# Kernel optimization log

Hardware: AMD Instinct MI355X
Metric: run time of the kernel (lower is better)

Reference implementation:

```python
import jax, jax.numpy as jnp
import numpy as np

N = 100000
E = 3200000
G = 64  # number of graphs


def _lin_params(key, fan_in, fan_out):
    k1, k2 = jax.random.split(key)
    bound = 1.0 / np.sqrt(fan_in)
    W = jax.random.uniform(k1, (fan_in, fan_out), jnp.float32, -bound, bound)
    b = jax.random.uniform(k2, (fan_out,), jnp.float32, -bound, bound)
    return W, b


def setup_inputs() -> dict:
    key = jax.random.key(0)
    ks = jax.random.split(key, 12)
    x = jax.random.normal(ks[0], (N, 3), jnp.float32)
    edge_index = jax.random.randint(ks[1], (2, E), 0, N, jnp.int32)
    batch = jnp.sort(jax.random.randint(ks[2], (N,), 0, G, jnp.int32))
    # conv1: in=3, heads=4, out_channels=16, concat=True -> 64
    Wq1, bq1 = _lin_params(ks[3], 3, 64)
    Wk1, bk1 = _lin_params(ks[4], 3, 64)
    Wv1, bv1 = _lin_params(ks[5], 3, 64)
    Ws1, bs1 = _lin_params(ks[6], 3, 64)
    # conv2: in=64, heads=1, out_channels=6, concat=False -> 6
    Wq2, bq2 = _lin_params(ks[7], 64, 6)
    Wk2, bk2 = _lin_params(ks[8], 64, 6)
    Wv2, bv2 = _lin_params(ks[9], 64, 6)
    Ws2, bs2 = _lin_params(ks[10], 64, 6)
    return dict(x=x, edge_index=edge_index, batch=batch,
                Wq1=Wq1, bq1=bq1, Wk1=Wk1, bk1=bk1, Wv1=Wv1, bv1=bv1, Ws1=Ws1, bs1=bs1,
                Wq2=Wq2, bq2=bq2, Wk2=Wk2, bk2=bk2, Wv2=Wv2, bv2=bv2, Ws2=Ws2, bs2=bs2)


def transformer_conv(x, src, dst, Wq, bq, Wk, bk, Wv, bv, Ws, bs, heads, d, concat):
    n = x.shape[0]
    q = (x @ Wq + bq).reshape(n, heads, d)
    k = (x @ Wk + bk).reshape(n, heads, d)
    v = (x @ Wv + bv).reshape(n, heads, d)
    # per-edge attention logits: query at target, key at source  [E, H]
    logits = jnp.einsum('ehd,ehd->eh', q[dst], k[src]) / jnp.sqrt(jnp.float32(d))
    # segment softmax over incoming edges of each target node
    m = jax.ops.segment_max(logits, dst, num_segments=n)          # [N, H]
    a = jnp.exp(logits - m[dst])                                   # [E, H]
    denom = jax.ops.segment_sum(a, dst, num_segments=n)           # [N, H]
    alpha = a / (denom[dst] + 1e-16)
    out = jax.ops.segment_sum(alpha[:, :, None] * v[src], dst, num_segments=n)  # [N,H,d]
    out = out.reshape(n, heads * d) if concat else out.mean(axis=1)
    return out + x @ Ws + bs  # root/skip connection


def reference(x, edge_index, batch,
              Wq1, bq1, Wk1, bk1, Wv1, bv1, Ws1, bs1,
              Wq2, bq2, Wk2, bk2, Wv2, bv2, Ws2, bs2):
    src, dst = edge_index[0], edge_index[1]
    h = transformer_conv(x, src, dst, Wq1, bq1, Wk1, bk1, Wv1, bv1, Ws1, bs1,
                         heads=4, d=16, concat=True)
    h = jax.nn.relu(h)
    # dropout is identity in eval mode
    h = transformer_conv(h, src, dst, Wq2, bq2, Wk2, bk2, Wv2, bv2, Ws2, bs2,
                         heads=1, d=6, concat=False)
    # global mean pool over graphs
    sums = jax.ops.segment_sum(h, batch, num_segments=G)
    cnts = jax.ops.segment_sum(jnp.ones((h.shape[0],), h.dtype), batch, num_segments=G)
    pooled = sums / jnp.maximum(cnts, 1.0)[:, None]
    return jax.nn.log_softmax(pooled, axis=1)
```

## Files before the change

### kernel.cpp

```cpp
#include <hip/hip_runtime.h>
#include <hip/hip_fp16.h>
#include <math.h>

#define N_NODES 100000
#define N_EDGES 3200000
#define N_GRAPHS 64
#define NEG_INF -1e30f

#define NB 196
#define CAP 18432
#define NBLK 512
#define CHUNK 6250

__device__ __forceinline__ void atomAddF(float* p, float v) {
#if defined(__HIP_PLATFORM_AMD__)
    unsafeAtomicAdd(p, v);
#else
    atomicAdd(p, v);
#endif
}

__device__ __forceinline__ float b2f(unsigned w, int sh) {
    return (float)(signed char)(w >> sh);
}

__device__ __forceinline__ float kvdot(const float* q, uint4 w, float* sv_out) {
    float2 s = __half22float2(*(const __half2*)&w.w);
    *sv_out = s.y;
    return s.x * (q[0] * b2f(w.x, 0) + q[1] * b2f(w.x, 8)
                + q[2] * b2f(w.x, 16) + q[3] * b2f(w.x, 24)
                + q[4] * b2f(w.y, 0) + q[5] * b2f(w.y, 8));
}

__global__ void k0_packx(const float* __restrict__ x, float4* __restrict__ xp,
                         uint2* __restrict__ xh) {
    int n = blockIdx.x * 256 + threadIdx.x;
    if (n >= N_NODES) return;
    float x0 = x[3 * n], x1 = x[3 * n + 1], x2 = x[3 * n + 2];
    xp[n] = make_float4(x0, x1, x2, 0.f);
    __half2 h01 = __floats2half2_rn(x0, x1);
    __half2 h2p = __floats2half2_rn(x2, 0.f);
    xh[n] = make_uint2(*(unsigned*)&h01, *(unsigned*)&h2p);
}

__global__ __launch_bounds__(512) void s1_partition(const int* __restrict__ ei,
                                                    int* __restrict__ offs,
                                                    unsigned* __restrict__ pairs) {
    __shared__ unsigned pairbuf[CHUNK];
    __shared__ unsigned sortbuf[CHUNK];
    __shared__ unsigned char buckbuf[CHUNK];
    __shared__ int hist[8][200];
    __shared__ int cur[NB], tmp[NB];
    int tid = threadIdx.x;
    int wp = tid >> 6;
    for (int i = tid; i < 8 * 200; i += 512) ((int*)hist)[i] = 0;
    __syncthreads();
    int gbase = blockIdx.x * CHUNK;
    for (int i = tid; i < CHUNK; i += 512) {
        int src = ei[gbase + i];
        unsigned dst = (unsigned)ei[N_EDGES + gbase + i];
        pairbuf[i] = ((unsigned)src << 9) | (dst & 511u);
        unsigned b = dst >> 9;
        buckbuf[i] = (unsigned char)b;
        atomicAdd(&hist[wp][b], 1);
    }
    __syncthreads();
    if (tid < NB) {
        int s = 0;
#pragma unroll
        for (int w = 0; w < 8; ++w) s += hist[w][tid];
        tmp[tid] = s;
        hist[0][tid] = s;
    }
    __syncthreads();
    for (int off = 1; off < NB; off <<= 1) {
        int v = 0;
        if (tid < NB && tid >= off) v = tmp[tid - off];
        __syncthreads();
        if (tid < NB) tmp[tid] += v;
        __syncthreads();
    }
    if (tid < NB) {
        int excl = tmp[tid] - hist[0][tid];
        cur[tid] = excl;
        offs[blockIdx.x * NB + tid] = excl;
    }
    __syncthreads();
    for (int i = tid; i < CHUNK; i += 512) {
        int pos = atomicAdd(&cur[buckbuf[i]], 1);
        sortbuf[pos] = pairbuf[i];
    }
    __syncthreads();
    for (int i = tid; i < CHUNK; i += 512)
        pairs[gbase + i] = sortbuf[i];
}

#define B4T 1024
__global__ __launch_bounds__(B4T) void b4_build(const unsigned* __restrict__ pairs,
                                                const int* __restrict__ offs,
                                                int* __restrict__ rs,
                                                int* __restrict__ re,
                                                int* __restrict__ csr_src) {
    __shared__ unsigned eLDS[CAP];
    __shared__ int so[NBLK], slen[NBLK], dbase[NBLK];
    __shared__ int cnt2[2][512];
    __shared__ int sc[512], cur[512];
    int b = blockIdx.x;
    int tid = threadIdx.x;

    for (int k = tid; k < NBLK; k += B4T) {
        int s = offs[k * NB + b];
        int e = (b == NB - 1) ? CHUNK : offs[k * NB + b + 1];
        so[k] = s;
        slen[k] = e - s;
    }
    ((int*)cnt2)[tid] = 0;
    __syncthreads();
    if (tid < NBLK) sc[tid] = slen[tid];
    __syncthreads();
    for (int off = 1; off < NBLK; off <<= 1) {
        int v = (tid < NBLK && tid >= off) ? sc[tid - off] : 0;
        __syncthreads();
        if (tid < NBLK) sc[tid] += v;
        __syncthreads();
    }
    if (tid < NBLK) dbase[tid] = sc[tid] - slen[tid];
    __syncthreads();
    int ne = dbase[NBLK - 1] + slen[NBLK - 1];

    int wave = tid >> 6, lane = tid & 63;
    for (int k = wave; k < NBLK; k += (B4T / 64)) {
        int gb = k * CHUNK + so[k];
        int db = dbase[k], ln = slen[k];
        for (int i = lane; i < ln; i += 64)
            eLDS[db + i] = pairs[gb + i];
    }
    __syncthreads();

    int half = tid >> 9;
    for (int i = tid; i < ne; i += B4T)
        atomicAdd(&cnt2[half][eLDS[i] & 511u], 1);
    __syncthreads();
    int mycnt = 0;
    if (tid < 512) {
        mycnt = cnt2[0][tid] + cnt2[1][tid];
        sc[tid] = mycnt;
    }
    __syncthreads();
    for (int off = 1; off < 512; off <<= 1) {
        int v = (tid < 512 && tid >= off) ? sc[tid - off] : 0;
        __syncthreads();
        if (tid < 512) sc[tid] += v;
        __syncthreads();
    }
    int rbase = b * CAP;
    if (tid < 512) {
        int excl = sc[tid] - mycnt;
        cur[tid] = rbase + excl;
        int node = (b << 9) + tid;
        if (node < N_NODES) {
            rs[node] = rbase + excl;
            re[node] = rbase + sc[tid];
        }
    }
    __syncthreads();
    for (int i = tid; i < ne; i += B4T) {
        unsigned p = eLDS[i];
        int pos = atomicAdd(&cur[p & 511u], 1);
        csr_src[pos] = (int)(p >> 9);
    }
}

__global__ void g1_layer1(const float4* __restrict__ xp,
                          const uint2* __restrict__ xh,
                          const float* __restrict__ Wq, const float* __restrict__ bq,
                          const float* __restrict__ Wk, const float* __restrict__ bk,
                          const float* __restrict__ Wv, const float* __restrict__ bv,
                          const float* __restrict__ Ws, const float* __restrict__ bs,
                          const int* __restrict__ rs, const int* __restrict__ re,
                          const int* __restrict__ csr_src,
                          uint2* __restrict__ h1) {
    __shared__ float sWq[192], sWk[192], sWv[192], sWs[192];
    __shared__ float sbq[64], sbk[64], sbv[64], sbs[64];
    for (int i = threadIdx.x; i < 192; i += 256) {
        sWq[i] = Wq[i]; sWk[i] = Wk[i]; sWv[i] = Wv[i]; sWs[i] = Ws[i];
    }
    for (int i = threadIdx.x; i < 64; i += 256) {
        sbq[i] = bq[i]; sbk[i] = bk[i]; sbv[i] = bv[i]; sbs[i] = bs[i];
    }
    __syncthreads();

    int lane = threadIdx.x & 63;
    int u = lane & 15;
    int slot = u >> 2;
    int j0 = u * 4;
    int n = blockIdx.x * 16 + (threadIdx.x >> 6) * 4 + (lane >> 4);

    float4 xc = xp[n];
    float x0 = xc.x, x1 = xc.y, x2 = xc.z;

    float q[4];
#pragma unroll
    for (int i = 0; i < 4; ++i)
        q[i] = 0.25f * (sbq[j0 + i] + x0 * sWq[j0 + i] + x1 * sWq[64 + j0 + i]
                        + x2 * sWq[128 + j0 + i]);
    float t0 = 0.f, t1 = 0.f, t2 = 0.f, tb = 0.f;
#pragma unroll
    for (int i = 0; i < 4; ++i) {
        float qi = q[i];
        t0 += qi * sWk[j0 + i];
        t1 += qi * sWk[64 + j0 + i];
        t2 += qi * sWk[128 + j0 + i];
        tb += qi * sbk[j0 + i];
    }
#pragma unroll
    for (int off = 1; off <= 2; off <<= 1) {
        t0 += __shfl_xor(t0, off);
        t1 += __shfl_xor(t1, off);
        t2 += __shfl_xor(t2, off);
        tb += __shfl_xor(tb, off);
    }
    int tsrc = (lane & 48) | ((lane & 3) << 2) | ((lane >> 2) & 3);
    t0 = __shfl(t0, tsrc, 64);
    t1 = __shfl(t1, tsrc, 64);
    t2 = __shfl(t2, tsrc, 64);
    tb = __shfl(tb, tsrc, 64);

    int row = rs[n];
    int deg = re[n] - row;

    float mA = NEG_INF, dA = 0.f, s0A = 0.f, s1A = 0.f, s2A = 0.f;
    float mB = NEG_INF, dB = 0.f, s0B = 0.f, s1B = 0.f, s2B = 0.f;
    for (int base = 0; base < deg; base += 8) {
        int eA = base + slot, eB = base + 4 + slot;
        bool vA = eA < deg, vB = eB < deg;
        int srcA = vA ? csr_src[row + eA] : 0;
        int srcB = vB ? csr_src[row + eB] : 0;
        uint2 wA = xh[srcA];
        uint2 wB = xh[srcB];
        float2 a01 = __half22float2(*(const __half2*)&wA.x);
        float a2 = __half22float2(*(const __half2*)&wA.y).x;
        float2 b01 = __half22float2(*(const __half2*)&wB.x);
        float b2 = __half22float2(*(const __half2*)&wB.y).x;
        float lA = vA ? (tb + a01.x * t0 + a01.y * t1 + a2 * t2) : NEG_INF;
        float lB = vB ? (tb + b01.x * t0 + b01.y * t1 + b2 * t2) : NEG_INF;
        float mnA = fmaxf(mA, lA);
        float scA = __expf(mA - mnA);
        float aA = vA ? __expf(lA - mnA) : 0.f;
        dA = dA * scA + aA;
        s0A = s0A * scA + aA * a01.x;
        s1A = s1A * scA + aA * a01.y;
        s2A = s2A * scA + aA * a2;
        mA = mnA;
        float mnB = fmaxf(mB, lB);
        float scB = __expf(mB - mnB);
        float aB = vB ? __expf(lB - mnB) : 0.f;
        dB = dB * scB + aB;
        s0B = s0B * scB + aB * b01.x;
        s1B = s1B * scB + aB * b01.y;
        s2B = s2B * scB + aB * b2;
        mB = mnB;
    }
    float m = fmaxf(mA, mB);
    float fA = __expf(mA - m), fB = __expf(mB - m);
    float d = dA * fA + dB * fB;
    float s0 = s0A * fA + s0B * fB;
    float s1 = s1A * fA + s1B * fB;
    float s2 = s2A * fA + s2B * fB;

    float gm = m;
    gm = fmaxf(gm, __shfl_xor(gm, 4));
    gm = fmaxf(gm, __shfl_xor(gm, 8));
    float f = __expf(m - gm);
    d *= f; s0 *= f; s1 *= f; s2 *= f;
#pragma unroll
    for (int off = 4; off <= 8; off <<= 1) {
        d += __shfl_xor(d, off);
        s0 += __shfl_xor(s0, off);
        s1 += __shfl_xor(s1, off);
        s2 += __shfl_xor(s2, off);
    }

    int esrc = (lane & 48) | ((lane >> 2) & 3);
    float dH = __shfl(d, esrc, 64);
    float s0H = __shfl(s0, esrc, 64);
    float s1H = __shfl(s1, esrc, 64);
    float s2H = __shfl(s2, esrc, 64);
    float inv = 1.f / (dH + 1e-16f);
    float fr = dH * inv, r0 = s0H * inv, r1 = s1H * inv, r2 = s2H * inv;

    float o[4];
#pragma unroll
    for (int i = 0; i < 4; ++i) {
        int j = j0 + i;
        float val = fr * sbv[j] + r0 * sWv[j] + r1 * sWv[64 + j] + r2 * sWv[128 + j]
                  + sbs[j] + x0 * sWs[j] + x1 * sWs[64 + j] + x2 * sWs[128 + j];
        o[i] = fmaxf(val, 0.f);
    }
    __half2 p01 = __floats2half2_rn(o[0], o[1]);
    __half2 p23 = __floats2half2_rn(o[2], o[3]);
    h1[(size_t)n * 16 + u] = make_uint2(*(unsigned*)&p01, *(unsigned*)&p23);
}

__global__ void k5_node2(const unsigned* __restrict__ h1,
                         const float* __restrict__ Wq, const float* __restrict__ bq,
                         const float* __restrict__ Wk, const float* __restrict__ bk,
                         const float* __restrict__ Wv, const float* __restrict__ bv,
                         const float* __restrict__ Ws, const float* __restrict__ bs,
                         uint4* __restrict__ q2h, float* __restrict__ s2,
                         uint4* __restrict__ kv2) {
    __shared__ float sWq[384], sWk[384], sWv[384], sWs[384];
    __shared__ float sbq[6], sbk[6], sbv[6], sbs[6];
    for (int i = threadIdx.x; i < 384; i += blockDim.x) {
        sWq[i] = Wq[i]; sWk[i] = Wk[i]; sWv[i] = Wv[i]; sWs[i] = Ws[i];
    }
    if (threadIdx.x < 6) {
        sbq[threadIdx.x] = bq[threadIdx.x];
        sbk[threadIdx.x] = bk[threadIdx.x];
        sbv[threadIdx.x] = bv[threadIdx.x];
        sbs[threadIdx.x] = bs[threadIdx.x];
    }
    __syncthreads();
    int n = blockIdx.x * blockDim.x + threadIdx.x;
    if (n >= N_NODES) return;
    float qa[6], ka[6], va[6], sa[6];
#pragma unroll
    for (int c = 0; c < 6; ++c) { qa[c] = sbq[c]; ka[c] = sbk[c]; va[c] = sbv[c]; sa[c] = sbs[c]; }
    const uint4* hp = reinterpret_cast<const uint4*>(h1 + (size_t)n * 32);
#pragma unroll
    for (int i4 = 0; i4 < 8; ++i4) {
        uint4 hv = hp[i4];
        float2 f01 = __half22float2(*(const __half2*)&hv.x);
        float2 f23 = __half22float2(*(const __half2*)&hv.y);
        float2 f45 = __half22float2(*(const __half2*)&hv.z);
        float2 f67 = __half22float2(*(const __half2*)&hv.w);
        float hvv[8] = {f01.x, f01.y, f23.x, f23.y, f45.x, f45.y, f67.x, f67.y};
#pragma unroll
        for (int uu = 0; uu < 8; ++uu) {
            float hx = hvv[uu];
            int i = i4 * 8 + uu;
#pragma unroll
            for (int c = 0; c < 6; ++c) {
                qa[c] += hx * sWq[i * 6 + c];
                ka[c] += hx * sWk[i * 6 + c];
                va[c] += hx * sWv[i * 6 + c];
                sa[c] += hx * sWs[i * 6 + c];
            }
        }
    }
    const float rsqrt6 = 0.4082482904638631f;
    {
        __half2 h01 = __floats2half2_rn(qa[0] * rsqrt6, qa[1] * rsqrt6);
        __half2 h23 = __floats2half2_rn(qa[2] * rsqrt6, qa[3] * rsqrt6);
        __half2 h45 = __floats2half2_rn(qa[4] * rsqrt6, qa[5] * rsqrt6);
        uint4 w;
        w.x = *(unsigned*)&h01; w.y = *(unsigned*)&h23;
        w.z = *(unsigned*)&h45; w.w = 0u;
        q2h[n] = w;
    }
#pragma unroll
    for (int c = 0; c < 6; ++c) s2[(size_t)n * 6 + c] = sa[c];
    float mk = 0.f, mv = 0.f;
#pragma unroll
    for (int c = 0; c < 6; ++c) {
        mk = fmaxf(mk, fabsf(ka[c]));
        mv = fmaxf(mv, fabsf(va[c]));
    }
    float sk = fmaxf(mk, 1e-8f) * (1.f / 127.f);
    float sv = fmaxf(mv, 1e-8f) * (1.f / 127.f);
    float isk = 1.f / sk, isv = 1.f / sv;
    int qk[6], qv[6];
#pragma unroll
    for (int c = 0; c < 6; ++c) {
        qk[c] = __float2int_rn(ka[c] * isk);
        qv[c] = __float2int_rn(va[c] * isv);
    }
    uint4 w;
    w.x = (qk[0] & 255) | ((qk[1] & 255) << 8) | ((qk[2] & 255) << 16) | ((qk[3] & 255) << 24);
    w.y = (qk[4] & 255) | ((qk[5] & 255) << 8) | ((qv[0] & 255) << 16) | ((qv[1] & 255) << 24);
    w.z = (qv[2] & 255) | ((qv[3] & 255) << 8) | ((qv[4] & 255) << 16) | ((qv[5] & 255) << 24);
    __half2 hs = __floats2half2_rn(sk, sv);
    w.w = *(unsigned*)&hs;
    kv2[n] = w;
}

__global__ void g2_layer2(const int* __restrict__ rs, const int* __restrict__ re,
                          const int* __restrict__ csr_src,
                          const uint4* __restrict__ q2h,
                          const uint4* __restrict__ kv2,
                          const float* __restrict__ s2,
                          const int* __restrict__ batch,
                          float* __restrict__ psum, float* __restrict__ pcnt) {
    __shared__ float bsum[N_GRAPHS * 6];
    __shared__ float bcnt[N_GRAPHS];
    for (int i = threadIdx.x; i < N_GRAPHS * 6; i += 256) bsum[i] = 0.f;
    for (int i = threadIdx.x; i < N_GRAPHS; i += 256) bcnt[i] = 0.f;
    __syncthreads();

    int node = blockIdx.x * 32 + (threadIdx.x >> 3);
    int lane8 = threadIdx.x & 7;

    uint4 qw = q2h[node];
    float2 q01 = __half22float2(*(const __half2*)&qw.x);
    float2 q23 = __half22float2(*(const __half2*)&qw.y);
    float2 q45 = __half22float2(*(const __half2*)&qw.z);
    float q[6] = {q01.x, q01.y, q23.x, q23.y, q45.x, q45.y};
    int row = rs[node];
    int deg = re[node] - row;

    float lg[8], svr[8];
    unsigned py[8], pz[8];
#pragma unroll
    for (int i = 0; i < 8; ++i) { lg[i] = NEG_INF; svr[i] = 0.f; py[i] = 0u; pz[i] = 0u; }
    float lmax = NEG_INF;
#pragma unroll
    for (int i = 0; i < 4; ++i) {
        int e = lane8 + i * 8;
        bool v = e < deg;
        int src = v ? csr_src[row + e] : 0;
        uint4 w = kv2[src];
        float svx;
        float l = kvdot(q, w, &svx);
        if (v) {
            lg[i] = l; svr[i] = svx; py[i] = w.y; pz[i] = w.z;
            lmax = fmaxf(lmax, l);
        }
    }
    if (deg > 32) {
#pragma unroll
        for (int i = 4; i < 8; ++i) {
            int e = lane8 + i * 8;
            bool v = e < deg;
            int src = v ? csr_src[row + e] : 0;
            uint4 w = kv2[src];
            float svx;
            float l = kvdot(q, w, &svx);
            if (v) {
                lg[i] = l; svr[i] = svx; py[i] = w.y; pz[i] = w.z;
                lmax = fmaxf(lmax, l);
            }
        }
    }
    float mo = NEG_INF, dov = 0.f;
    float ao[6] = {0.f, 0.f, 0.f, 0.f, 0.f, 0.f};
    for (int e = lane8 + 64; e < deg; e += 8) {
        int src = csr_src[row + e];
        uint4 w = kv2[src];
        float svx;
        float l = kvdot(q, w, &svx);
        float mn = fmaxf(mo, l);
        float scp = __expf(mo - mn);
        float wx = __expf(l - mn);
        float wsx = wx * svx;
        dov = dov * scp + wx;
        ao[0] = ao[0] * scp + wsx * b2f(w.y, 16);
        ao[1] = ao[1] * scp + wsx * b2f(w.y, 24);
        ao[2] = ao[2] * scp + wsx * b2f(w.z, 0);
        ao[3] = ao[3] * scp + wsx * b2f(w.z, 8);
        ao[4] = ao[4] * scp + wsx * b2f(w.z, 16);
        ao[5] = ao[5] * scp + wsx * b2f(w.z, 24);
        mo = mn;
    }
    lmax = fmaxf(lmax, mo);
    lmax = fmaxf(lmax, __shfl_xor(lmax, 1));
    lmax = fmaxf(lmax, __shfl_xor(lmax, 2));
    lmax = fmaxf(lmax, __shfl_xor(lmax, 4));
    if (lmax < -5e29f) lmax = 0.f;

    float d = 0.f;
    float acc[6] = {0.f, 0.f, 0.f, 0.f, 0.f, 0.f};
#pragma unroll
    for (int i = 0; i < 8; ++i) {
        float w = __expf(lg[i] - lmax);
        float ws = w * svr[i];
        d += w;
        acc[0] += ws * b2f(py[i], 16);
        acc[1] += ws * b2f(py[i], 24);
        acc[2] += ws * b2f(pz[i], 0);
        acc[3] += ws * b2f(pz[i], 8);
        acc[4] += ws * b2f(pz[i], 16);
        acc[5] += ws * b2f(pz[i], 24);
    }
    float so = __expf(mo - lmax);
    d += dov * so;
#pragma unroll
    for (int c = 0; c < 6; ++c) acc[c] += ao[c] * so;

#pragma unroll
    for (int off = 1; off <= 4; off <<= 1) {
        d += __shfl_xor(d, off);
#pragma unroll
        for (int c = 0; c < 6; ++c) acc[c] += __shfl_xor(acc[c], off);
    }

    if (lane8 == 0) {
        float inv = 1.f / (d + 1e-16f);
        int g = batch[node];
#pragma unroll
        for (int c = 0; c < 6; ++c) {
            float val = acc[c] * inv + s2[(size_t)node * 6 + c];
            atomicAdd(&bsum[g * 6 + c], val);
        }
        atomicAdd(&bcnt[g], 1.f);
    }
    __syncthreads();
    for (int i = threadIdx.x; i < N_GRAPHS * 6; i += 256) {
        float v = bsum[i];
        if (v != 0.f) atomAddF(psum + i, v);
    }
    for (int i = threadIdx.x; i < N_GRAPHS; i += 256) {
        float v = bcnt[i];
        if (v != 0.f) atomAddF(pcnt + i, v);
    }
}

__global__ void k9_final(const float* __restrict__ psum, const float* __restrict__ pcnt,
                         float* __restrict__ out) {
    int g = threadIdx.x;
    if (g >= N_GRAPHS) return;
    float cnt = fmaxf(pcnt[g], 1.0f);
    float z[6];
    float mx = -1e30f;
#pragma unroll
    for (int c = 0; c < 6; ++c) {
        z[c] = psum[g * 6 + c] / cnt;
        mx = fmaxf(mx, z[c]);
    }
    float se = 0.f;
#pragma unroll
    for (int c = 0; c < 6; ++c) se += __expf(z[c] - mx);
    float lse = mx + logf(se);
#pragma unroll
    for (int c = 0; c < 6; ++c) out[g * 6 + c] = z[c] - lse;
}

extern "C" void kernel_launch(void* const* d_in, const int* in_sizes, int n_in,
                              void* d_out, int out_size, void* d_ws, size_t ws_size,
                              hipStream_t stream) {
    const float* x   = (const float*)d_in[0];
    const int*   ei  = (const int*)d_in[1];
    const int*   bat = (const int*)d_in[2];
    const float* Wq1 = (const float*)d_in[3];  const float* bq1 = (const float*)d_in[4];
    const float* Wk1 = (const float*)d_in[5];  const float* bk1 = (const float*)d_in[6];
    const float* Wv1 = (const float*)d_in[7];  const float* bv1 = (const float*)d_in[8];
    const float* Ws1 = (const float*)d_in[9];  const float* bs1 = (const float*)d_in[10];
    const float* Wq2 = (const float*)d_in[11]; const float* bq2 = (const float*)d_in[12];
    const float* Wk2 = (const float*)d_in[13]; const float* bk2 = (const float*)d_in[14];
    const float* Wv2 = (const float*)d_in[15]; const float* bv2 = (const float*)d_in[16];
    const float* Ws2 = (const float*)d_in[17]; const float* bs2 = (const float*)d_in[18];
    float* out = (float*)d_out;

    char* ws = (char*)d_ws;
    size_t off = 0;
    auto alloc = [&](size_t bytes) -> char* {
        char* p = ws + off;
        off += (bytes + 255) & ~(size_t)255;
        return p;
    };

    float* psum = (float*)alloc((size_t)N_GRAPHS * 6 * 4);
    float* pcnt = (float*)alloc((size_t)N_GRAPHS * 4);
    size_t zero_bytes = off;

    int*      offs    = (int*)     alloc((size_t)NBLK * NB * 4);
    unsigned* pairs   = (unsigned*)alloc((size_t)N_EDGES * 4);
    int*      csr_src = (int*)     alloc((size_t)NB * CAP * 4);
    int*      rsv     = (int*)     alloc((size_t)N_NODES * 4);
    int*      rev     = (int*)     alloc((size_t)N_NODES * 4);
    float4*   xp      = (float4*)  alloc((size_t)N_NODES * 16);
    uint2*    xh      = (uint2*)   alloc((size_t)N_NODES * 8);
    unsigned* h1      = (unsigned*)alloc((size_t)N_NODES * 64 * 2);
    uint4*    q2h     = (uint4*)   alloc((size_t)N_NODES * 16);
    float*    s2      = (float*)   alloc((size_t)N_NODES * 6 * 4);
    uint4*    kv2     = (uint4*)   alloc((size_t)N_NODES * 16);

    hipMemsetAsync(d_ws, 0, zero_bytes, stream);

    k0_packx<<<(N_NODES + 255) / 256, 256, 0, stream>>>(x, xp, xh);
    s1_partition<<<NBLK, 512, 0, stream>>>(ei, offs, pairs);
    b4_build<<<NB, B4T, 0, stream>>>(pairs, offs, rsv, rev, csr_src);

    g1_layer1<<<N_NODES / 16, 256, 0, stream>>>(xp, xh, Wq1, bq1, Wk1, bk1, Wv1, bv1,
                                                Ws1, bs1, rsv, rev, csr_src,
                                                (uint2*)h1);
    k5_node2<<<(N_NODES + 255) / 256, 256, 0, stream>>>(h1, Wq2, bq2, Wk2, bk2,
                                                        Wv2, bv2, Ws2, bs2,
                                                        q2h, s2, kv2);
    g2_layer2<<<N_NODES / 32, 256, 0, stream>>>(rsv, rev, csr_src, q2h, kv2, s2,
                                                bat, psum, pcnt);
    k9_final<<<1, 64, 0, stream>>>(psum, pcnt, out);
}
```

Measured before the change: 142.4 us.

## Fold pack, memset and final softmax into neighbouring kernels

Moves the x packing and the psum/pcnt zeroing into the partition kernel, with 512 blocks of 196 nodes each covering all 100000 nodes. It also replaces the separate log-softmax kernel with a last-block-done pattern at the end of layer2, using an atomic counter and thread fences. This removes one memset and two kernel launches and their inter-kernel gaps, at the cost of an extra atomic and fence per layer2 block.

```diff
diff --git a/kernel.cpp b/kernel.cpp
--- a/kernel.cpp
+++ b/kernel.cpp
@@ -32,18 +32,13 @@
                 + q[4] * b2f(w.y, 0) + q[5] * b2f(w.y, 8));
 }
 
-__global__ void k0_packx(const float* __restrict__ x, float4* __restrict__ xp,
-                         uint2* __restrict__ xh) {
-    int n = blockIdx.x * 256 + threadIdx.x;
-    if (n >= N_NODES) return;
-    float x0 = x[3 * n], x1 = x[3 * n + 1], x2 = x[3 * n + 2];
-    xp[n] = make_float4(x0, x1, x2, 0.f);
-    __half2 h01 = __floats2half2_rn(x0, x1);
-    __half2 h2p = __floats2half2_rn(x2, 0.f);
-    xh[n] = make_uint2(*(unsigned*)&h01, *(unsigned*)&h2p);
-}
-
 __global__ __launch_bounds__(512) void s1_partition(const int* __restrict__ ei,
+                                                    const float* __restrict__ x,
+                                                    float4* __restrict__ xp,
+                                                    uint2* __restrict__ xh,
+                                                    float* __restrict__ psum,
+                                                    float* __restrict__ pcnt,
+                                                    int* __restrict__ done,
                                                     int* __restrict__ offs,
                                                     unsigned* __restrict__ pairs) {
     __shared__ unsigned pairbuf[CHUNK];
@@ -52,6 +47,23 @@
     __shared__ int hist[8][200];
     __shared__ int cur[NB], tmp[NB];
     int tid = threadIdx.x;
+
+    {
+        int n = blockIdx.x * 196 + tid;
+        if (tid < 196 && n < N_NODES) {
+            float x0 = x[3 * n], x1 = x[3 * n + 1], x2 = x[3 * n + 2];
+            xp[n] = make_float4(x0, x1, x2, 0.f);
+            __half2 h01 = __floats2half2_rn(x0, x1);
+            __half2 h2p = __floats2half2_rn(x2, 0.f);
+            xh[n] = make_uint2(*(unsigned*)&h01, *(unsigned*)&h2p);
+        }
+    }
+    if (blockIdx.x == 0) {
+        for (int i = tid; i < N_GRAPHS * 6; i += 512) psum[i] = 0.f;
+        for (int i = tid; i < N_GRAPHS; i += 512) pcnt[i] = 0.f;
+        if (tid == 0) *done = 0;
+    }
+
     int wp = tid >> 6;
     for (int i = tid; i < 8 * 200; i += 512) ((int*)hist)[i] = 0;
     __syncthreads();
@@ -390,9 +402,11 @@
                           const uint4* __restrict__ kv2,
                           const float* __restrict__ s2,
                           const int* __restrict__ batch,
-                          float* __restrict__ psum, float* __restrict__ pcnt) {
+                          float* __restrict__ psum, float* __restrict__ pcnt,
+                          int* __restrict__ done, float* __restrict__ out) {
     __shared__ float bsum[N_GRAPHS * 6];
     __shared__ float bcnt[N_GRAPHS];
+    __shared__ int isLast;
     for (int i = threadIdx.x; i < N_GRAPHS * 6; i += 256) bsum[i] = 0.f;
     for (int i = threadIdx.x; i < N_GRAPHS; i += 256) bcnt[i] = 0.f;
     __syncthreads();
@@ -512,26 +526,34 @@
         float v = bcnt[i];
         if (v != 0.f) atomAddF(pcnt + i, v);
     }
-}
-
-__global__ void k9_final(const float* __restrict__ psum, const float* __restrict__ pcnt,
-                         float* __restrict__ out) {
-    int g = threadIdx.x;
-    if (g >= N_GRAPHS) return;
-    float cnt = fmaxf(pcnt[g], 1.0f);
-    float z[6];
-    float mx = -1e30f;
-#pragma unroll
-    for (int c = 0; c < 6; ++c) {
-        z[c] = psum[g * 6 + c] / cnt;
-        mx = fmaxf(mx, z[c]);
-    }
-    float se = 0.f;
-#pragma unroll
-    for (int c = 0; c < 6; ++c) se += __expf(z[c] - mx);
-    float lse = mx + logf(se);
-#pragma unroll
-    for (int c = 0; c < 6; ++c) out[g * 6 + c] = z[c] - lse;
+
+    __threadfence();
+    __syncthreads();
+    if (threadIdx.x == 0) {
+        int prev = atomicAdd(done, 1);
+        isLast = (prev == (int)gridDim.x - 1) ? 1 : 0;
+    }
+    __syncthreads();
+    if (isLast) {
+        __threadfence();
+        int g = threadIdx.x;
+        if (g < N_GRAPHS) {
+            float cnt = fmaxf(pcnt[g], 1.0f);
+            float z[6];
+            float mx = -1e30f;
+#pragma unroll
+            for (int c = 0; c < 6; ++c) {
+                z[c] = psum[g * 6 + c] / cnt;
+                mx = fmaxf(mx, z[c]);
+            }
+            float se = 0.f;
+#pragma unroll
+            for (int c = 0; c < 6; ++c) se += __expf(z[c] - mx);
+            float lse = mx + logf(se);
+#pragma unroll
+            for (int c = 0; c < 6; ++c) out[g * 6 + c] = z[c] - lse;
+        }
+    }
 }
 
 extern "C" void kernel_launch(void* const* d_in, const int* in_sizes, int n_in,
@@ -558,10 +580,9 @@
         return p;
     };
 
-    float* psum = (float*)alloc((size_t)N_GRAPHS * 6 * 4);
-    float* pcnt = (float*)alloc((size_t)N_GRAPHS * 4);
-    size_t zero_bytes = off;
-
+    float*    psum    = (float*)   alloc((size_t)N_GRAPHS * 6 * 4);
+    float*    pcnt    = (float*)   alloc((size_t)N_GRAPHS * 4);
+    int*      done    = (int*)     alloc(256);
     int*      offs    = (int*)     alloc((size_t)NBLK * NB * 4);
     unsigned* pairs   = (unsigned*)alloc((size_t)N_EDGES * 4);
     int*      csr_src = (int*)     alloc((size_t)NB * CAP * 4);
@@ -574,10 +595,8 @@
     float*    s2      = (float*)   alloc((size_t)N_NODES * 6 * 4);
     uint4*    kv2     = (uint4*)   alloc((size_t)N_NODES * 16);
 
-    hipMemsetAsync(d_ws, 0, zero_bytes, stream);
-
-    k0_packx<<<(N_NODES + 255) / 256, 256, 0, stream>>>(x, xp, xh);
-    s1_partition<<<NBLK, 512, 0, stream>>>(ei, offs, pairs);
+    s1_partition<<<NBLK, 512, 0, stream>>>(ei, x, xp, xh, psum, pcnt, done,
+                                           offs, pairs);
     b4_build<<<NB, B4T, 0, stream>>>(pairs, offs, rsv, rev, csr_src);
 
     g1_layer1<<<N_NODES / 16, 256, 0, stream>>>(xp, xh, Wq1, bq1, Wk1, bk1, Wv1, bv1,
@@ -587,6 +606,5 @@
                                                         Wv2, bv2, Ws2, bs2,
                                                         q2h, s2, kv2);
     g2_layer2<<<N_NODES / 32, 256, 0, stream>>>(rsv, rev, csr_src, q2h, kv2, s2,
-                                                bat, psum, pcnt);
-    k9_final<<<1, 64, 0, stream>>>(psum, pcnt, out);
-}
+                                                bat, psum, pcnt, done, out);
+}
```

After: 313.7 us. 2.2x slower.
